# Performance work log

Hardware: AMD Instinct MI355X
Metric: run time of the kernel (lower is better)

The kernel has to match this reference:

```python
import jax, jax.numpy as jnp
import numpy as np

B, T, D = 2, 1024, 1024
H = 8            # num_heads
DK = 128         # head_k_dim
DV = 128         # head_v_dim
M = 128          # num_slots (== head_k_dim by default)
K = 32           # topk
EPS = 1e-5
SCALE = 1.0


def _rmsnorm(x, w, eps=EPS):
    return x * jax.lax.rsqrt(jnp.mean(x * x, axis=-1, keepdims=True) + eps) * w


def setup_inputs() -> dict:
    key = jax.random.key(0)
    ks = jax.random.split(key, 12)
    def lin(k, fan_in, fan_out):
        return jax.random.normal(k, (fan_in, fan_out), jnp.float32) / np.sqrt(fan_in).astype(np.float32)
    hidden_states = jax.random.normal(ks[0], (B, T, D), jnp.float32)
    Wq = lin(ks[1], D, H * DK)
    Wk = lin(ks[2], D, H * DK)
    Wv = lin(ks[3], D, H * DV)
    Wr = lin(ks[4], D, H * M)
    Wa = lin(ks[5], D, H)
    # Mamba2-style decay params
    A_log = jnp.log(jax.random.uniform(ks[6], (H,), jnp.float32, 1e-3, 16.0))
    dt = jnp.exp(jax.random.uniform(ks[7], (H,), jnp.float32) * (np.log(0.1) - np.log(0.001)) + np.log(0.001))
    dt = jnp.clip(dt, 1e-4, None)
    dt_bias = dt + jnp.log(-jnp.expm1(-dt))
    q_norm_w = jnp.ones((DK,), jnp.float32) + 0.01 * jax.random.normal(ks[8], (DK,), jnp.float32)
    k_norm_w = jnp.ones((DK,), jnp.float32) + 0.01 * jax.random.normal(ks[9], (DK,), jnp.float32)
    g_norm_w = jnp.ones((D,), jnp.float32) + 0.01 * jax.random.normal(ks[10], (D,), jnp.float32)
    Wo = lin(ks[11], H * DV, D)
    return dict(hidden_states=hidden_states, Wq=Wq, Wk=Wk, Wv=Wv, Wr=Wr, Wa=Wa,
                A_log=A_log, dt_bias=dt_bias, q_norm_w=q_norm_w, k_norm_w=k_norm_w,
                g_norm_w=g_norm_w, Wo=Wo)


def reference(hidden_states, Wq, Wk, Wv, Wr, Wa, A_log, dt_bias, q_norm_w, k_norm_w, g_norm_w, Wo):
    b, t, d = hidden_states.shape
    # projections
    q = (hidden_states @ Wq).reshape(b, t, H, DK)
    k = (hidden_states @ Wk).reshape(b, t, H, DK)
    v = jax.nn.silu((hidden_states @ Wv).reshape(b, t, H, DV))
    router = (hidden_states @ Wr).reshape(b, t, H, M)
    # Mamba2 decay (log-space, per head)
    f_head = -jnp.exp(A_log) * jax.nn.softplus(hidden_states @ Wa + dt_bias)  # [b,t,H]
    # swish feature map + per-head RMSNorm
    q = _rmsnorm(jax.nn.silu(q), q_norm_w)
    k = _rmsnorm(jax.nn.silu(k), k_norm_w)
    # sigmoid router scores, top-k slot routing (eval: no gumbel noise)
    scores = jax.nn.sigmoid(router)                    # [b,t,H,M]
    top_w, top_i = jax.lax.top_k(scores, K)            # [b,t,H,K]
    top_w = top_w / (jnp.sum(top_w, axis=-1, keepdims=True) + 1e-9)
    n = b * t * H
    rows = jnp.arange(n)[:, None]
    s_multihot = jnp.zeros((n, M), scores.dtype).at[rows, top_i.reshape(n, K)].set(
        top_w.reshape(n, K)).reshape(b, t, H, M)
    f = f_head[..., None] * s_multihot                 # [b,t,H,M], log decay per slot
    s = 1.0 - jnp.exp(f)                               # write gate per slot
    # decayed linear-attention recurrence over slots (M == DK):
    #   S_t[i,j] = exp(f_t[i]) * S_{t-1}[i,j] + s_t[i]*k_t[i]*v_t[j]
    #   o_t[j]   = scale * sum_i q_t[i] * S_t[i,j]
    def step(S, xs):
        q_t, k_t, v_t, f_t, s_t = xs                   # [b,H,*]
        S = jnp.exp(f_t)[..., None] * S + (s_t * k_t)[..., None] * v_t[..., None, :]
        o_t = jnp.einsum('bhk,bhkv->bhv', q_t, S) * SCALE
        return S, o_t
    xs = tuple(jnp.swapaxes(a, 0, 1) for a in (q, k, v, f, s))  # time-major
    S0 = jnp.zeros((b, H, DK, DV), q.dtype)
    _, o = jax.lax.scan(step, S0, xs)                  # o: [t,b,H,DV]
    o = jnp.swapaxes(o, 0, 1).reshape(b, t, H * DV)
    o = _rmsnorm(o, g_norm_w)                          # g_norm over hidden_size
    return o @ Wo
```

## Files before the change

### kernel.cpp

```cpp
#include <hip/hip_runtime.h>
#include <stdint.h>
#include <stddef.h>

#define H_ 8
#define T_ 1024

typedef __attribute__((ext_vector_type(8))) short s16x8;
typedef __attribute__((ext_vector_type(4))) float f32x4;
typedef __attribute__((ext_vector_type(16))) float f32x16;

static __device__ __forceinline__ unsigned short f2bf(float f){
  unsigned u = __float_as_uint(f);
  u += 0x7fffu + ((u >> 16) & 1u);
  return (unsigned short)(u >> 16);
}
static __device__ __forceinline__ float bf2f(unsigned short b){
  return __uint_as_float(((unsigned)b) << 16);
}
static __device__ __forceinline__ unsigned int pack_hl(float x){
  unsigned short h = f2bf(x);
  unsigned short l = f2bf(x - bf2f(h));
  return ((unsigned int)h << 16) | l;
}
static __device__ __forceinline__ void gl_lds16(const unsigned short* g, unsigned short* l){
  __builtin_amdgcn_global_load_lds((const __attribute__((address_space(1))) unsigned int*)g,
                                   (__attribute__((address_space(3))) unsigned int*)l,
                                   16, 0, 0);
}

__global__ void prep_k(const float* __restrict__ X, const float* __restrict__ Wa,
                       const float* __restrict__ A_log, const float* __restrict__ dtb,
                       unsigned short* __restrict__ hi, unsigned short* __restrict__ lo,
                       float* __restrict__ fh){
  __shared__ float xs[1024];
  int n = blockIdx.x, tid = threadIdx.x;
  size_t base = (size_t)n*1024 + tid*4;
  float4 x = *(const float4*)&X[base];
  *(float4*)&xs[tid*4] = x;
  float v[4] = {x.x,x.y,x.z,x.w};
  ushort4 h4, l4;
  unsigned short hh[4], ll[4];
#pragma unroll
  for(int j=0;j<4;j++){ hh[j]=f2bf(v[j]); ll[j]=f2bf(v[j]-bf2f(hh[j])); }
  h4.x=hh[0];h4.y=hh[1];h4.z=hh[2];h4.w=hh[3];
  l4.x=ll[0];l4.y=ll[1];l4.z=ll[2];l4.w=ll[3];
  *(ushort4*)&hi[base] = h4;
  *(ushort4*)&lo[base] = l4;
  __syncthreads();
  int h = tid>>5, l = tid&31;
  float s = 0.f;
  for(int k=l;k<1024;k+=32) s += xs[k]*Wa[(size_t)k*8 + h];
  s += __shfl_xor(s,1); s += __shfl_xor(s,2); s += __shfl_xor(s,4);
  s += __shfl_xor(s,8); s += __shfl_xor(s,16);
  if(l==0){
    float z = s + dtb[h];
    float sp = (z > 20.f) ? z : log1pf(expf(z));
    fh[(size_t)n*8 + h] = -expf(A_log[h]) * sp;
  }
}

__global__ void wtrans(const float* __restrict__ Wq, const float* __restrict__ Wk,
                       const float* __restrict__ Wv, const float* __restrict__ Wr,
                       const float* __restrict__ Wo,
                       unsigned short* __restrict__ WcatT3, unsigned short* __restrict__ WrThi,
                       unsigned short* __restrict__ WrTlo, unsigned short* __restrict__ WoT){
  __shared__ float tile[32][33];
  int z = blockIdx.z;
  const float* src = (z==0)?Wq:(z==1)?Wk:(z==2)?Wv:(z==3)?Wr:Wo;
  int c0 = blockIdx.x*32;
  int k0 = blockIdx.y*32;
  int tx = threadIdx.x, ty = threadIdx.y;
#pragma unroll
  for(int r=0;r<32;r+=8)
    tile[ty+r][tx] = src[(size_t)(k0+ty+r)*1024 + c0 + tx];
  __syncthreads();
#pragma unroll
  for(int r=0;r<32;r+=8){
    int c = c0 + ty + r;
    int k = k0 + tx;
    float v = tile[tx][ty+r];
    if(z < 3){
      WcatT3[((size_t)(z*1024 + c))*1024 + k] = f2bf(v);
    } else if(z == 3){
      unsigned short hv = f2bf(v);
      WrThi[(size_t)c*1024 + k] = hv;
      WrTlo[(size_t)c*1024 + k] = f2bf(v - bf2f(hv));
    } else {
      WoT[(size_t)c*1024 + k] = f2bf(v);
    }
  }
}

__launch_bounds__(256)
__global__ void gemm_fused(const unsigned short* __restrict__ Xhi, const unsigned short* __restrict__ Xlo,
                           const unsigned short* __restrict__ WcatT3, const unsigned short* __restrict__ WrThi,
                           const unsigned short* __restrict__ WrTlo,
                           float* __restrict__ C1, float* __restrict__ Rp){
  __shared__ unsigned short As[128*64];
  __shared__ unsigned short Bs[128*64];
  int bid = blockIdx.x;
  int blk = (bid&7)*96 + (bid>>3);
  const unsigned short *Ap, *Bp;
  float* Cout;
  int bx, by, N;
  if(blk < 384){
    bx = blk%24; by = blk/24; N = 3072;
    Ap = Xhi; Bp = WcatT3; Cout = C1;
  } else {
    int rb = blk-384;
    int seg = rb>>7, t2 = rb&127;
    bx = t2&7; by = t2>>3; N = 1024;
    Ap = (seg==2) ? Xlo : Xhi;
    Bp = (seg==1) ? WrTlo : WrThi;
    Cout = Rp + (size_t)seg*2048*1024;
  }
  int tid = threadIdx.x;
  int mBase = by*128, nBase = bx*128;
  int w = tid>>6, lane = tid&63, wr = w>>1, wc = w&1;
  int kg = lane>>4, l15 = lane&15;
  f32x4 acc[4][4];
#pragma unroll
  for(int i=0;i<4;i++)
#pragma unroll
    for(int j=0;j<4;j++) acc[i][j] = (f32x4){0.f,0.f,0.f,0.f};
  size_t aoff[4], boff[4];
#pragma unroll
  for(int p=0;p<4;p++){
    int c = p*256 + tid;
    int row = c>>3, sc = c&7, c8 = sc ^ (row&7);
    aoff[p] = (size_t)(mBase+row)*1024 + c8*8;
    boff[p] = (size_t)(nBase+row)*1024 + c8*8;
  }
  for(int kb=0; kb<1024; kb+=64){
#pragma unroll
    for(int p=0;p<4;p++){
      gl_lds16(Ap + aoff[p] + kb, &As[(p*256+tid)*8]);
      gl_lds16(Bp + boff[p] + kb, &Bs[(p*256+tid)*8]);
    }
    __syncthreads();
#pragma unroll
    for(int kk=0;kk<2;kk++){
      s16x8 afr[4], bfr[4];
#pragma unroll
      for(int f=0;f<4;f++){
        int rA = wr*64 + f*16 + l15;
        int rB = wc*64 + f*16 + l15;
        int cA = (kk*4 + kg) ^ (rA&7);
        int cB = (kk*4 + kg) ^ (rB&7);
        afr[f] = *(const s16x8*)&As[rA*64 + cA*8];
        bfr[f] = *(const s16x8*)&Bs[rB*64 + cB*8];
      }
#pragma unroll
      for(int fm=0;fm<4;fm++)
#pragma unroll
        for(int fn=0;fn<4;fn++)
          acc[fm][fn] = __builtin_amdgcn_mfma_f32_16x16x32_bf16(afr[fm], bfr[fn], acc[fm][fn], 0,0,0);
    }
    __syncthreads();
  }
#pragma unroll
  for(int fm=0;fm<4;fm++)
#pragma unroll
    for(int fn=0;fn<4;fn++){
      int col = nBase + wc*64 + fn*16 + l15;
      int row = mBase + wr*64 + fm*16 + kg*4;
#pragma unroll
      for(int r=0;r<4;r++) Cout[(size_t)(row+r)*N + col] = acc[fm][fn][r];
    }
}

__launch_bounds__(256)
__global__ void gemm_out(const unsigned short* __restrict__ A,
                         const unsigned short* __restrict__ BT,
                         float* __restrict__ C){
  __shared__ unsigned short As[128*64];
  __shared__ unsigned short Bs[64*64];
  const int K = 1024, N = 1024;
  int tid = threadIdx.x;
  int mBase = blockIdx.y*128, nBase = blockIdx.x*64;
  int w = tid>>6, lane = tid&63;
  int mh = w>>1, nh = w&1;
  int kg = lane>>4, l15 = lane&15;
  f32x4 acc[4][2];
#pragma unroll
  for(int i=0;i<4;i++)
#pragma unroll
    for(int j=0;j<2;j++) acc[i][j] = (f32x4){0.f,0.f,0.f,0.f};
  size_t aoff[4], boff[2];
#pragma unroll
  for(int p=0;p<4;p++){
    int c = p*256 + tid;
    int row = c>>3, sc = c&7, c8 = sc ^ (row&7);
    aoff[p] = (size_t)(mBase+row)*K + c8*8;
  }
#pragma unroll
  for(int p=0;p<2;p++){
    int c = p*256 + tid;
    int row = c>>3, sc = c&7, c8 = sc ^ (row&7);
    boff[p] = (size_t)(nBase+row)*K + c8*8;
  }
  for(int kb=0; kb<K; kb+=64){
#pragma unroll
    for(int p=0;p<4;p++) gl_lds16(A + aoff[p] + kb, &As[(p*256+tid)*8]);
#pragma unroll
    for(int p=0;p<2;p++) gl_lds16(BT + boff[p] + kb, &Bs[(p*256+tid)*8]);
    __syncthreads();
#pragma unroll
    for(int kk=0;kk<2;kk++){
      s16x8 afr[4], bfr[2];
#pragma unroll
      for(int f=0;f<4;f++){
        int r = mh*64 + f*16 + l15;
        afr[f] = *(const s16x8*)&As[r*64 + ((kk*4+kg) ^ (r&7))*8];
      }
#pragma unroll
      for(int f=0;f<2;f++){
        int r = nh*32 + f*16 + l15;
        bfr[f] = *(const s16x8*)&Bs[r*64 + ((kk*4+kg) ^ (r&7))*8];
      }
#pragma unroll
      for(int fm=0;fm<4;fm++)
#pragma unroll
        for(int fn=0;fn<2;fn++)
          acc[fm][fn] = __builtin_amdgcn_mfma_f32_16x16x32_bf16(afr[fm], bfr[fn], acc[fm][fn], 0,0,0);
    }
    __syncthreads();
  }
#pragma unroll
  for(int fm=0;fm<4;fm++)
#pragma unroll
    for(int fn=0;fn<2;fn++){
      int col = nBase + nh*32 + fn*16 + l15;
      int row = mBase + mh*64 + fm*16 + kg*4;
#pragma unroll
      for(int r=0;r<4;r++) C[(size_t)(row+r)*N + col] = acc[fm][fn][r];
    }
}

__launch_bounds__(256)
__global__ void pp_sum(const float* __restrict__ C1, const float* __restrict__ Rp,
                       const float* __restrict__ fh, const float* __restrict__ qw,
                       const float* __restrict__ kw,
                       float* __restrict__ Qd, float* __restrict__ Wt,
                       float* __restrict__ Fd, float* __restrict__ Vd,
                       float* __restrict__ dS, float* __restrict__ E){
  __shared__ unsigned scU[32][128];
  __shared__ float Fc[32][132];
  __shared__ float Kh[32][132];
  __shared__ float Vs[32][132];
  int blk = blockIdx.x, bh = blk>>5, c = blk&31;
  int b = bh>>3, h = bh&7;
  int tid = threadIdx.x;
  int g = tid>>5, i0 = (tid&31)*4;
  int n0 = b*1024 + c*32;
  size_t fbase = ((size_t)bh*T_ + (size_t)c*32)*128;
  float si_r[4][4];
  unsigned ki_r[4][4];
#pragma unroll
  for(int v=0; v<4; v++){
    int t2 = v*8 + g;
    size_t rb = (size_t)(n0 + t2)*1024 + h*128 + i0;
    float4 r0 = *(const float4*)&Rp[rb];
    float4 r1 = *(const float4*)&Rp[2048ull*1024 + rb];
    float4 r2 = *(const float4*)&Rp[2ull*2048*1024 + rb];
    float rl[4] = {r0.x+r1.x+r2.x, r0.y+r1.y+r2.y, r0.z+r1.z+r2.z, r0.w+r1.w+r2.w};
#pragma unroll
    for(int j=0;j<4;j++){
      float si = 1.f/(1.f+expf(-rl[j]));
      si_r[v][j] = si;
      ki_r[v][j] = (__float_as_uint(si) & ~127u) | (unsigned)(127 - (i0+j));
      scU[t2][i0+j] = ki_r[v][j];
    }
  }
  __syncthreads();
#pragma unroll
  for(int v=0; v<4; v++){
    int t2 = v*8 + g;
    int n = n0 + t2;
    size_t cb = (size_t)n*3072 + h*128 + i0;
    float4 q4 = *(const float4*)&C1[cb];
    float4 k4 = *(const float4*)&C1[cb + 1024];
    float4 v4 = *(const float4*)&C1[cb + 2048];
    float qv[4]={q4.x,q4.y,q4.z,q4.w}, kv[4]={k4.x,k4.y,k4.z,k4.w}, vraw[4]={v4.x,v4.y,v4.z,v4.w};
    float qs[4], ks[4], vv[4];
#pragma unroll
    for(int j=0;j<4;j++){
      qs[j] = qv[j]/(1.f+expf(-qv[j]));
      ks[j] = kv[j]/(1.f+expf(-kv[j]));
      vv[j] = vraw[j]/(1.f+expf(-vraw[j]));
    }
    int cnt[4]={0,0,0,0};
#pragma unroll 4
    for(int j=0;j<128;j+=4){
      uint4 kk4 = *(const uint4*)&scU[t2][j];
      unsigned kk[4]={kk4.x,kk4.y,kk4.z,kk4.w};
#pragma unroll
      for(int m=0;m<4;m++)
        cnt[m] += (int)(kk[0]>ki_r[v][m]) + (int)(kk[1]>ki_r[v][m])
                + (int)(kk[2]>ki_r[v][m]) + (int)(kk[3]>ki_r[v][m]);
    }
    bool sel[4];
#pragma unroll
    for(int m=0;m<4;m++) sel[m] = cnt[m] < 32;
    float x;
    x = qs[0]*qs[0]+qs[1]*qs[1]+qs[2]*qs[2]+qs[3]*qs[3];
    x+=__shfl_xor(x,1);x+=__shfl_xor(x,2);x+=__shfl_xor(x,4);x+=__shfl_xor(x,8);x+=__shfl_xor(x,16);
    float qrms = rsqrtf(x/128.f + 1e-5f);
    x = ks[0]*ks[0]+ks[1]*ks[1]+ks[2]*ks[2]+ks[3]*ks[3];
    x+=__shfl_xor(x,1);x+=__shfl_xor(x,2);x+=__shfl_xor(x,4);x+=__shfl_xor(x,8);x+=__shfl_xor(x,16);
    float krms = rsqrtf(x/128.f + 1e-5f);
    x = (sel[0]?si_r[v][0]:0.f)+(sel[1]?si_r[v][1]:0.f)+(sel[2]?si_r[v][2]:0.f)+(sel[3]?si_r[v][3]:0.f);
    x+=__shfl_xor(x,1);x+=__shfl_xor(x,2);x+=__shfl_xor(x,4);x+=__shfl_xor(x,8);x+=__shfl_xor(x,16);
    float winv = 1.f/(x + 1e-9f);
    float fhv = fh[(size_t)n*8 + h];
    float qd[4], wd[4], fd[4];
#pragma unroll
    for(int j=0;j<4;j++){
      float wgt = sel[j] ? si_r[v][j]*winv : 0.f;
      float f = fhv * wgt;
      qd[j] = qs[j]*qrms*qw[i0+j];
      wd[j] = (1.f - expf(f)) * (ks[j]*krms*kw[i0+j]);
      fd[j] = f;
    }
    size_t basev = fbase + (size_t)t2*128 + i0;
    float4 qo; qo.x=qd[0];qo.y=qd[1];qo.z=qd[2];qo.w=qd[3];
    float4 wo; wo.x=wd[0];wo.y=wd[1];wo.z=wd[2];wo.w=wd[3];
    float4 vo; vo.x=vv[0];vo.y=vv[1];vo.z=vv[2];vo.w=vv[3];
    *(float4*)&Qd[basev] = qo;
    *(float4*)&Wt[basev] = wo;
    *(float4*)&Vd[basev] = vo;
    *(float4*)&Fc[t2][i0] = make_float4(fd[0],fd[1],fd[2],fd[3]);
    *(float4*)&Kh[t2][i0] = wo;
    *(float4*)&Vs[t2][i0] = vo;
  }
  __syncthreads();
  if(tid < 128){
    float a = 0.f;
    for(int t2=0;t2<32;t2++){ a += Fc[t2][tid]; Fc[t2][tid] = a; }
  }
  __syncthreads();
#pragma unroll
  for(int v=0; v<4; v++){
    int e = v*1024 + tid*4;
    int t2 = e>>7, i2 = e&127;
    float4 fc4 = *(const float4*)&Fc[t2][i2];
    *(float4*)&Fd[fbase + e] = fc4;
    float4 ft  = *(const float4*)&Fc[31][i2];
    float4 kh  = *(const float4*)&Kh[t2][i2];
    kh.x *= expf(ft.x - fc4.x);
    kh.y *= expf(ft.y - fc4.y);
    kh.z *= expf(ft.z - fc4.z);
    kh.w *= expf(ft.w - fc4.w);
    *(float4*)&Kh[t2][i2] = kh;
  }
  if(tid < 128) E[((size_t)bh*32 + c)*128 + tid] = expf(Fc[31][tid]);
  __syncthreads();
  int w = tid>>6, lane = tid&63;
  int ig = lane>>3, jg = lane&7;
  f32x4 acc[4][4];
#pragma unroll
  for(int a=0;a<4;a++)
#pragma unroll
    for(int q=0;q<4;q++) acc[a][q] = (f32x4){0.f,0.f,0.f,0.f};
#pragma unroll 4
  for(int t2=0;t2<32;t2++){
    float4 kq = *(const float4*)&Kh[t2][w*32 + ig*4];
    float4 v0 = *(const float4*)&Vs[t2][jg*4];
    float4 v1 = *(const float4*)&Vs[t2][jg*4 + 32];
    float4 v2 = *(const float4*)&Vs[t2][jg*4 + 64];
    float4 v3 = *(const float4*)&Vs[t2][jg*4 + 96];
    float kk[4] = {kq.x,kq.y,kq.z,kq.w};
#pragma unroll
    for(int a=0;a<4;a++){
      acc[a][0] += kk[a]*(f32x4){v0.x,v0.y,v0.z,v0.w};
      acc[a][1] += kk[a]*(f32x4){v1.x,v1.y,v1.z,v1.w};
      acc[a][2] += kk[a]*(f32x4){v2.x,v2.y,v2.z,v2.w};
      acc[a][3] += kk[a]*(f32x4){v3.x,v3.y,v3.z,v3.w};
    }
  }
  size_t dbase = (size_t)blk*16384;
#pragma unroll
  for(int q=0;q<4;q++)
#pragma unroll
    for(int jj=0;jj<4;jj++){
      float4 o4 = make_float4(acc[0][q][jj],acc[1][q][jj],acc[2][q][jj],acc[3][q][jj]);
      *(float4*)&dS[dbase + (size_t)(jg*4 + 32*q + jj)*128 + w*32 + ig*4] = o4;
    }
}

__global__ void scan_k(float* __restrict__ dS, const float* __restrict__ E){
  int g = blockIdx.x*256 + threadIdx.x;
  int bh = g>>12;
  int e4 = (g&4095)*4;
  int i0 = e4 & 127;
  size_t base  = (size_t)bh*32*16384 + e4;
  size_t ebase = (size_t)bh*32*128 + i0;
  float4 S = make_float4(0.f,0.f,0.f,0.f);
  float4 d  = *(const float4*)&dS[base];
  float4 Ec = *(const float4*)&E[ebase];
  for(int c=0;c<32;c++){
    float4 dn = make_float4(0,0,0,0), En = make_float4(0,0,0,0);
    if(c < 31){
      dn = *(const float4*)&dS[base + (size_t)(c+1)*16384];
      En = *(const float4*)&E[ebase + (size_t)(c+1)*128];
    }
    *(float4*)&dS[base + (size_t)c*16384] = S;
    S.x = Ec.x*S.x + d.x;
    S.y = Ec.y*S.y + d.y;
    S.z = Ec.z*S.z + d.z;
    S.w = Ec.w*S.w + d.w;
    d = dn; Ec = En;
  }
}

__launch_bounds__(256)
__global__ void chunk_out(const float* __restrict__ Qd, const float* __restrict__ Wt,
                          const float* __restrict__ Fd, const float* __restrict__ Vd,
                          const float* __restrict__ ST, float* __restrict__ O){
  __shared__ unsigned int qtP[32][132];
  __shared__ unsigned int ktP[32][132];
  __shared__ unsigned int Vt[128][36];
  __shared__ float Amat[32][40];
  int blk = blockIdx.x, bh = blk>>5, c = blk&31;
  int b = bh>>3, h = bh&7;
  int tid = threadIdx.x, w = tid>>6, lane = tid&63;
  int m = lane&31, hi = lane>>5;
  size_t fbase = ((size_t)bh*T_ + (size_t)c*32)*128;
#pragma unroll
  for(int p=0;p<4;p++){
    int e = p*1024 + tid*4;
    int t2 = e>>7, i0 = e&127;
    float4 f4 = *(const float4*)&Fd[fbase + e];
    float4 q4 = *(const float4*)&Qd[fbase + e];
    float4 w4 = *(const float4*)&Wt[fbase + e];
    float fv[4] = {f4.x,f4.y,f4.z,f4.w};
    float qv[4] = {q4.x,q4.y,q4.z,q4.w};
    float wv[4] = {w4.x,w4.y,w4.z,w4.w};
    uint4 qp, kp;
    unsigned int qa[4], ka[4];
#pragma unroll
    for(int j=0;j<4;j++){
      float ef = expf(fv[j]);
      qa[j] = pack_hl(qv[j]*ef);
      ka[j] = pack_hl(wv[j]/ef);
    }
    qp.x=qa[0]; qp.y=qa[1]; qp.z=qa[2]; qp.w=qa[3];
    kp.x=ka[0]; kp.y=ka[1]; kp.z=ka[2]; kp.w=ka[3];
    *(uint4*)&qtP[t2][i0] = qp;
    *(uint4*)&ktP[t2][i0] = kp;
  }
  {
    int n = tid&127, th = (tid>>7)*16;
    unsigned int vp[16];
#pragma unroll
    for(int j=0;j<16;j++) vp[j] = pack_hl(Vd[fbase + (size_t)(th+j)*128 + n]);
#pragma unroll
    for(int j=0;j<16;j+=4){
      uint4 v4; v4.x=vp[j]; v4.y=vp[j+1]; v4.z=vp[j+2]; v4.w=vp[j+3];
      *(uint4*)&Vt[n][th+j] = v4;
    }
  }
  __syncthreads();
  if(w == 0){
    f32x16 am;
#pragma unroll
    for(int r=0;r<16;r++) am[r] = 0.f;
#pragma unroll
    for(int s=0;s<8;s++){
      int ko = s*16 + hi*8;
      uint4 qa = *(const uint4*)&qtP[m][ko];
      uint4 qb = *(const uint4*)&qtP[m][ko+4];
      uint4 ka = *(const uint4*)&ktP[m][ko];
      uint4 kb = *(const uint4*)&ktP[m][ko+4];
      s16x8 qh, ql, kh, kl;
      unsigned int qw_[8] = {qa.x,qa.y,qa.z,qa.w,qb.x,qb.y,qb.z,qb.w};
      unsigned int kw_[8] = {ka.x,ka.y,ka.z,ka.w,kb.x,kb.y,kb.z,kb.w};
#pragma unroll
      for(int j=0;j<8;j++){
        qh[j]=(short)(qw_[j]>>16); ql[j]=(short)(qw_[j]&0xffff);
        kh[j]=(short)(kw_[j]>>16); kl[j]=(short)(kw_[j]&0xffff);
      }
      am = __builtin_amdgcn_mfma_f32_32x32x16_bf16(qh, kh, am, 0,0,0);
      am = __builtin_amdgcn_mfma_f32_32x32x16_bf16(qh, kl, am, 0,0,0);
      am = __builtin_amdgcn_mfma_f32_32x32x16_bf16(ql, kh, am, 0,0,0);
    }
#pragma unroll
    for(int r=0;r<16;r++){
      int rm = (r&3) + 8*(r>>2) + 4*hi;
      Amat[rm][m] = (m <= rm) ? am[r] : 0.f;
    }
  }
  f32x16 oacc;
#pragma unroll
  for(int r=0;r<16;r++) oacc[r] = 0.f;
  const float* Sp = ST + (size_t)blk*16384 + (size_t)(w*32 + m)*128;
#pragma unroll
  for(int s=0;s<8;s++){
    int ko = s*16 + hi*8;
    uint4 qa = *(const uint4*)&qtP[m][ko];
    uint4 qb = *(const uint4*)&qtP[m][ko+4];
    s16x8 qh, ql;
    unsigned int qw_[8] = {qa.x,qa.y,qa.z,qa.w,qb.x,qb.y,qb.z,qb.w};
#pragma unroll
    for(int j=0;j<8;j++){ qh[j]=(short)(qw_[j]>>16); ql[j]=(short)(qw_[j]&0xffff); }
    float4 s0 = *(const float4*)&Sp[ko];
    float4 s1 = *(const float4*)&Sp[ko+4];
    float sv[8] = {s0.x,s0.y,s0.z,s0.w,s1.x,s1.y,s1.z,s1.w};
    s16x8 sh, sl;
#pragma unroll
    for(int j=0;j<8;j++){
      unsigned short hh = f2bf(sv[j]);
      sh[j] = (short)hh; sl[j] = (short)f2bf(sv[j]-bf2f(hh));
    }
    oacc = __builtin_amdgcn_mfma_f32_32x32x16_bf16(qh, sh, oacc, 0,0,0);
    oacc = __builtin_amdgcn_mfma_f32_32x32x16_bf16(qh, sl, oacc, 0,0,0);
    oacc = __builtin_amdgcn_mfma_f32_32x32x16_bf16(ql, sh, oacc, 0,0,0);
  }
  __syncthreads();
#pragma unroll
  for(int s=0;s<2;s++){
    int uo = s*16 + hi*8;
    float4 a0 = *(const float4*)&Amat[m][uo];
    float4 a1 = *(const float4*)&Amat[m][uo+4];
    float av[8] = {a0.x,a0.y,a0.z,a0.w,a1.x,a1.y,a1.z,a1.w};
    s16x8 ah, al;
#pragma unroll
    for(int j=0;j<8;j++){
      unsigned short hh = f2bf(av[j]);
      ah[j] = (short)hh; al[j] = (short)f2bf(av[j]-bf2f(hh));
    }
    uint4 v0 = *(const uint4*)&Vt[w*32 + m][uo];
    uint4 v1 = *(const uint4*)&Vt[w*32 + m][uo+4];
    unsigned int vw[8] = {v0.x,v0.y,v0.z,v0.w,v1.x,v1.y,v1.z,v1.w};
    s16x8 vh, vl;
#pragma unroll
    for(int j=0;j<8;j++){ vh[j]=(short)(vw[j]>>16); vl[j]=(short)(vw[j]&0xffff); }
    oacc = __builtin_amdgcn_mfma_f32_32x32x16_bf16(ah, vh, oacc, 0,0,0);
    oacc = __builtin_amdgcn_mfma_f32_32x32x16_bf16(ah, vl, oacc, 0,0,0);
    oacc = __builtin_amdgcn_mfma_f32_32x32x16_bf16(al, vh, oacc, 0,0,0);
  }
#pragma unroll
  for(int r=0;r<16;r++){
    int tok = (r&3) + 8*(r>>2) + 4*hi;
    O[((size_t)(b*T_ + c*32 + tok))*1024 + h*128 + w*32 + m] = oacc[r];
  }
}

__global__ void gnorm_k(const float* __restrict__ Ob, const float* __restrict__ gw,
                        unsigned short* __restrict__ On){
  __shared__ float red[4];
  int n = blockIdx.x, tid = threadIdx.x;
  size_t base = (size_t)n*1024 + tid*4;
  float4 x = *(const float4*)&Ob[base];
  float ss = x.x*x.x + x.y*x.y + x.z*x.z + x.w*x.w;
  ss+=__shfl_xor(ss,1);ss+=__shfl_xor(ss,2);ss+=__shfl_xor(ss,4);
  ss+=__shfl_xor(ss,8);ss+=__shfl_xor(ss,16);ss+=__shfl_xor(ss,32);
  if((tid&63)==0) red[tid>>6]=ss;
  __syncthreads();
  float sc = rsqrtf((red[0]+red[1]+red[2]+red[3])/1024.f + 1e-5f);
  float4 g = *(const float4*)&gw[tid*4];
  ushort4 o4;
  o4.x=f2bf(x.x*sc*g.x); o4.y=f2bf(x.y*sc*g.y);
  o4.z=f2bf(x.z*sc*g.z); o4.w=f2bf(x.w*sc*g.w);
  *(ushort4*)&On[base]=o4;
}

extern "C" void kernel_launch(void* const* d_in, const int* in_sizes, int n_in,
                              void* d_out, int out_size, void* d_ws, size_t ws_size,
                              hipStream_t stream){
  const float* hs   = (const float*)d_in[0];
  const float* Wq   = (const float*)d_in[1];
  const float* Wk   = (const float*)d_in[2];
  const float* Wv   = (const float*)d_in[3];
  const float* Wr   = (const float*)d_in[4];
  const float* Wa   = (const float*)d_in[5];
  const float* A_log= (const float*)d_in[6];
  const float* dtb  = (const float*)d_in[7];
  const float* qw   = (const float*)d_in[8];
  const float* kw   = (const float*)d_in[9];
  const float* gw   = (const float*)d_in[10];
  const float* Wo   = (const float*)d_in[11];
  float* out = (float*)d_out;

  char* wsp = (char*)d_ws;
  size_t off = 0;
  auto alloc = [&](size_t bytes)->void*{ void* p = wsp + off; off += (bytes + 255) & ~(size_t)255; return p; };
  unsigned short* Xhi    = (unsigned short*)alloc(2048ull*1024*2);
  unsigned short* Xlo    = (unsigned short*)alloc(2048ull*1024*2);
  unsigned short* WcatT3 = (unsigned short*)alloc(3072ull*1024*2);
  unsigned short* WrThi  = (unsigned short*)alloc(1024ull*1024*2);
  unsigned short* WrTlo  = (unsigned short*)alloc(1024ull*1024*2);
  unsigned short* WoT    = (unsigned short*)alloc(1024ull*1024*2);
  float* C1 = (float*)alloc(2048ull*3072*4);
  float* Rp = (float*)alloc(3ull*2048*1024*4);
  float* fh = (float*)alloc(2048ull*8*4);
  float* Qd = (float*)alloc(16ull*1024*128*4);
  float* Wt = (float*)alloc(16ull*1024*128*4);
  float* Fd = (float*)alloc(16ull*1024*128*4);
  float* Vd = (float*)alloc(16ull*1024*128*4);
  float* E  = (float*)alloc(16ull*32*128*4);
  float* dS = (float*)alloc(16ull*32*16384*4);
  float* Ob = (float*)alloc(2048ull*1024*4);
  unsigned short* On = (unsigned short*)alloc(2048ull*1024*2);
  (void)ws_size; (void)in_sizes; (void)n_in; (void)out_size;

  prep_k     <<<dim3(2048),        dim3(256),   0, stream>>>(hs, Wa, A_log, dtb, Xhi, Xlo, fh);
  wtrans     <<<dim3(32,32,5),     dim3(32,8),  0, stream>>>(Wq,Wk,Wv,Wr,Wo, WcatT3,WrThi,WrTlo,WoT);
  gemm_fused <<<dim3(768),         dim3(256),   0, stream>>>(Xhi, Xlo, WcatT3, WrThi, WrTlo, C1, Rp);
  pp_sum     <<<dim3(512),         dim3(256),   0, stream>>>(C1, Rp, fh, qw, kw, Qd, Wt, Fd, Vd, dS, E);
  scan_k     <<<dim3(256),         dim3(256),   0, stream>>>(dS, E);
  chunk_out  <<<dim3(512),         dim3(256),   0, stream>>>(Qd, Wt, Fd, Vd, dS, Ob);
  gnorm_k    <<<dim3(2048),        dim3(256),   0, stream>>>(Ob, gw, On);
  gemm_out   <<<dim3(16,16),       dim3(256),   0, stream>>>(On, WoT, out);
}
```

Baseline: 251.1 us.

## Compute chunk state outer product with split-bf16 MFMA in pp_sum

Replaces the FP32 scalar outer-product accumulation of the per-chunk state delta (K^T V over 32 timesteps) with 32x32x16 bf16 MFMA instructions. Each operand is split into a high and a low bf16 part, and three MFMAs recover near-fp32 accuracy. K and V values stay in registers and are written to LDS as packed hi/lo pairs. The router key buffer is aliased onto the V buffer to cut shared memory, and launch bounds request 3 blocks per CU. The risks are a small precision loss from dropping the lo*lo term and strided, uncoalesced scalar stores of the output.

```diff
diff --git a/kernel.cpp b/kernel.cpp
--- a/kernel.cpp
+++ b/kernel.cpp
@@ -237,17 +237,17 @@
     }
 }
 
-__launch_bounds__(256)
+__launch_bounds__(256, 3)
 __global__ void pp_sum(const float* __restrict__ C1, const float* __restrict__ Rp,
                        const float* __restrict__ fh, const float* __restrict__ qw,
                        const float* __restrict__ kw,
                        float* __restrict__ Qd, float* __restrict__ Wt,
                        float* __restrict__ Fd, float* __restrict__ Vd,
                        float* __restrict__ dS, float* __restrict__ E){
-  __shared__ unsigned scU[32][128];
   __shared__ float Fc[32][132];
-  __shared__ float Kh[32][132];
-  __shared__ float Vs[32][132];
+  __shared__ unsigned KhP[32][128];
+  __shared__ unsigned VsP[32][128];
+  unsigned (*scU)[128] = VsP;
   int blk = blockIdx.x, bh = blk>>5, c = blk&31;
   int b = bh>>3, h = bh&7;
   int tid = threadIdx.x;
@@ -273,6 +273,7 @@
     }
   }
   __syncthreads();
+  float wd_r[4][4], vv_r[4][4];
 #pragma unroll
   for(int v=0; v<4; v++){
     int t2 = v*8 + g;
@@ -282,12 +283,12 @@
     float4 k4 = *(const float4*)&C1[cb + 1024];
     float4 v4 = *(const float4*)&C1[cb + 2048];
     float qv[4]={q4.x,q4.y,q4.z,q4.w}, kv[4]={k4.x,k4.y,k4.z,k4.w}, vraw[4]={v4.x,v4.y,v4.z,v4.w};
-    float qs[4], ks[4], vv[4];
+    float qs[4], ks[4];
 #pragma unroll
     for(int j=0;j<4;j++){
       qs[j] = qv[j]/(1.f+expf(-qv[j]));
       ks[j] = kv[j]/(1.f+expf(-kv[j]));
-      vv[j] = vraw[j]/(1.f+expf(-vraw[j]));
+      vv_r[v][j] = vraw[j]/(1.f+expf(-vraw[j]));
     }
     int cnt[4]={0,0,0,0};
 #pragma unroll 4
@@ -313,25 +314,23 @@
     x+=__shfl_xor(x,1);x+=__shfl_xor(x,2);x+=__shfl_xor(x,4);x+=__shfl_xor(x,8);x+=__shfl_xor(x,16);
     float winv = 1.f/(x + 1e-9f);
     float fhv = fh[(size_t)n*8 + h];
-    float qd[4], wd[4], fd[4];
+    float qd[4], fd[4];
 #pragma unroll
     for(int j=0;j<4;j++){
       float wgt = sel[j] ? si_r[v][j]*winv : 0.f;
       float f = fhv * wgt;
       qd[j] = qs[j]*qrms*qw[i0+j];
-      wd[j] = (1.f - expf(f)) * (ks[j]*krms*kw[i0+j]);
+      wd_r[v][j] = (1.f - expf(f)) * (ks[j]*krms*kw[i0+j]);
       fd[j] = f;
     }
     size_t basev = fbase + (size_t)t2*128 + i0;
     float4 qo; qo.x=qd[0];qo.y=qd[1];qo.z=qd[2];qo.w=qd[3];
-    float4 wo; wo.x=wd[0];wo.y=wd[1];wo.z=wd[2];wo.w=wd[3];
-    float4 vo; vo.x=vv[0];vo.y=vv[1];vo.z=vv[2];vo.w=vv[3];
+    float4 wo; wo.x=wd_r[v][0];wo.y=wd_r[v][1];wo.z=wd_r[v][2];wo.w=wd_r[v][3];
+    float4 vo; vo.x=vv_r[v][0];vo.y=vv_r[v][1];vo.z=vv_r[v][2];vo.w=vv_r[v][3];
     *(float4*)&Qd[basev] = qo;
     *(float4*)&Wt[basev] = wo;
     *(float4*)&Vd[basev] = vo;
     *(float4*)&Fc[t2][i0] = make_float4(fd[0],fd[1],fd[2],fd[3]);
-    *(float4*)&Kh[t2][i0] = wo;
-    *(float4*)&Vs[t2][i0] = vo;
   }
   __syncthreads();
   if(tid < 128){
@@ -341,50 +340,61 @@
   __syncthreads();
 #pragma unroll
   for(int v=0; v<4; v++){
-    int e = v*1024 + tid*4;
-    int t2 = e>>7, i2 = e&127;
-    float4 fc4 = *(const float4*)&Fc[t2][i2];
-    *(float4*)&Fd[fbase + e] = fc4;
-    float4 ft  = *(const float4*)&Fc[31][i2];
-    float4 kh  = *(const float4*)&Kh[t2][i2];
-    kh.x *= expf(ft.x - fc4.x);
-    kh.y *= expf(ft.y - fc4.y);
-    kh.z *= expf(ft.z - fc4.z);
-    kh.w *= expf(ft.w - fc4.w);
-    *(float4*)&Kh[t2][i2] = kh;
+    int t2 = v*8 + g;
+    size_t basev = fbase + (size_t)t2*128 + i0;
+    float4 fc4 = *(const float4*)&Fc[t2][i0];
+    *(float4*)&Fd[basev] = fc4;
+    float4 ft = *(const float4*)&Fc[31][i0];
+    float fcv[4]={fc4.x,fc4.y,fc4.z,fc4.w}, ftv[4]={ft.x,ft.y,ft.z,ft.w};
+    unsigned kp[4], vp[4];
+#pragma unroll
+    for(int j=0;j<4;j++){
+      kp[j] = pack_hl(wd_r[v][j] * expf(ftv[j] - fcv[j]));
+      vp[j] = pack_hl(vv_r[v][j]);
+    }
+    uint4 k4u; k4u.x=kp[0];k4u.y=kp[1];k4u.z=kp[2];k4u.w=kp[3];
+    uint4 v4u; v4u.x=vp[0];v4u.y=vp[1];v4u.z=vp[2];v4u.w=vp[3];
+    *(uint4*)&KhP[t2][i0] = k4u;
+    *(uint4*)&VsP[t2][i0] = v4u;
   }
   if(tid < 128) E[((size_t)bh*32 + c)*128 + tid] = expf(Fc[31][tid]);
   __syncthreads();
   int w = tid>>6, lane = tid&63;
-  int ig = lane>>3, jg = lane&7;
-  f32x4 acc[4][4];
-#pragma unroll
-  for(int a=0;a<4;a++)
-#pragma unroll
-    for(int q=0;q<4;q++) acc[a][q] = (f32x4){0.f,0.f,0.f,0.f};
-#pragma unroll 4
-  for(int t2=0;t2<32;t2++){
-    float4 kq = *(const float4*)&Kh[t2][w*32 + ig*4];
-    float4 v0 = *(const float4*)&Vs[t2][jg*4];
-    float4 v1 = *(const float4*)&Vs[t2][jg*4 + 32];
-    float4 v2 = *(const float4*)&Vs[t2][jg*4 + 64];
-    float4 v3 = *(const float4*)&Vs[t2][jg*4 + 96];
-    float kk[4] = {kq.x,kq.y,kq.z,kq.w};
-#pragma unroll
-    for(int a=0;a<4;a++){
-      acc[a][0] += kk[a]*(f32x4){v0.x,v0.y,v0.z,v0.w};
-      acc[a][1] += kk[a]*(f32x4){v1.x,v1.y,v1.z,v1.w};
-      acc[a][2] += kk[a]*(f32x4){v2.x,v2.y,v2.z,v2.w};
-      acc[a][3] += kk[a]*(f32x4){v3.x,v3.y,v3.z,v3.w};
+  int m = lane&31, hi2 = lane>>5;
+  f32x16 acc[4];
+#pragma unroll
+  for(int it=0;it<4;it++)
+#pragma unroll
+    for(int r=0;r<16;r++) acc[it][r] = 0.f;
+#pragma unroll
+  for(int kh2=0; kh2<2; kh2++){
+    int kb = kh2*16 + hi2*8;
+    s16x8 ah, al;
+#pragma unroll
+    for(int jj=0;jj<8;jj++){
+      unsigned u = VsP[kb+jj][w*32 + m];
+      ah[jj] = (short)(u>>16); al[jj] = (short)(u&0xffff);
+    }
+#pragma unroll
+    for(int it=0;it<4;it++){
+      s16x8 bh_, bl_;
+#pragma unroll
+      for(int jj=0;jj<8;jj++){
+        unsigned u = KhP[kb+jj][it*32 + m];
+        bh_[jj] = (short)(u>>16); bl_[jj] = (short)(u&0xffff);
+      }
+      acc[it] = __builtin_amdgcn_mfma_f32_32x32x16_bf16(ah, bh_, acc[it], 0,0,0);
+      acc[it] = __builtin_amdgcn_mfma_f32_32x32x16_bf16(ah, bl_, acc[it], 0,0,0);
+      acc[it] = __builtin_amdgcn_mfma_f32_32x32x16_bf16(al, bh_, acc[it], 0,0,0);
     }
   }
   size_t dbase = (size_t)blk*16384;
 #pragma unroll
-  for(int q=0;q<4;q++)
-#pragma unroll
-    for(int jj=0;jj<4;jj++){
-      float4 o4 = make_float4(acc[0][q][jj],acc[1][q][jj],acc[2][q][jj],acc[3][q][jj]);
-      *(float4*)&dS[dbase + (size_t)(jg*4 + 32*q + jj)*128 + w*32 + ig*4] = o4;
+  for(int it=0;it<4;it++)
+#pragma unroll
+    for(int r=0;r<16;r++){
+      int ro = (r&3) + 8*(r>>2) + 4*hi2;
+      dS[dbase + (size_t)(w*32 + ro)*128 + it*32 + m] = acc[it][r];
     }
 }
 
```

Result: no change. 246.6 us (-1.8%).
